# Kernel tuning notes

Measured on AMD Instinct MI355X. Metric: run time of the kernel, lower is better.

Reference implementation:

```python
import jax, jax.numpy as jnp
import numpy as np

NUM_FIELDS = 64
DIM = 128
BATCH = 8192


def setup_inputs() -> dict:
    key = jax.random.key(0)
    k1, k2 = jax.random.split(key)
    inputs = jax.random.normal(k1, (BATCH, NUM_FIELDS * DIM), dtype=jnp.float32)
    field_weights = jax.random.normal(k2, (NUM_FIELDS, NUM_FIELDS), dtype=jnp.float32)
    return {"inputs": inputs, "field_weights": field_weights}


def reference(inputs, field_weights):
    B = inputs.shape[0]
    F = NUM_FIELDS
    D = inputs.shape[1] // F
    x = inputs.reshape(B, F, D)  # [B, F, D]
    # Gram matrix of field vectors: G[b,i,j] = <x_i, x_j>
    gram = jnp.einsum('bid,bjd->bij', x, x)  # [B, F, F]
    # Only pairs (i, j) with i < j contribute (itertools.combinations)
    upper = jnp.triu(jnp.ones((F, F), dtype=inputs.dtype), k=1)
    w = field_weights * upper  # [F, F]
    out = jnp.einsum('bij,ij->b', gram, w)  # sum over masked weighted pairs
    return out[:, None]  # [B, 1]
```

## Files before the change

kernel.cpp:

```cpp
#include <hip/hip_runtime.h>

#define NF 64
#define ND 128

typedef __attribute__((ext_vector_type(8))) short bf16x8;
typedef __attribute__((ext_vector_type(4))) float f32x4;

__device__ __forceinline__ short f2bf(float f) {
    union { float f; unsigned u; } v; v.f = f;
    unsigned r = (v.u + 0x7FFFu + ((v.u >> 16) & 1u)) >> 16;
    return (short)r;
}

__global__ __launch_bounds__(256, 4) void wfi_mfma(const float* __restrict__ x,
                                                   const float* __restrict__ w,
                                                   float* __restrict__ out,
                                                   int Btot) {
    const int tid  = threadIdx.x;
    const int wv   = tid >> 6;
    const int lane = tid & 63;
    const int lo   = lane & 15;
    const int hi   = lane >> 4;
    const int b    = blockIdx.x * 4 + wv;
    if (b >= Btot) return;

    bf16x8 afr[4][2];
#pragma unroll
    for (int jt = 0; jt < 4; ++jt) {
        const int j = jt * 16 + lo;
#pragma unroll
        for (int kt = 0; kt < 2; ++kt) {
#pragma unroll
            for (int e = 0; e < 8; ++e) {
                const int i = kt * 32 + hi * 8 + e;
                const float wval = (i < j) ? w[i * NF + j] : 0.f;
                afr[jt][kt][e] = f2bf(wval);
            }
        }
    }

    const float* __restrict__ xb = x + (size_t)b * (NF * ND);
    float res = 0.f;

#pragma unroll
    for (int dt = 0; dt < 8; ++dt) {
        const int d = dt * 16 + lo;

        bf16x8 bfr[2];
#pragma unroll
        for (int kt = 0; kt < 2; ++kt) {
#pragma unroll
            for (int e = 0; e < 8; ++e) {
                const int i = kt * 32 + hi * 8 + e;
                bfr[kt][e] = f2bf(xb[i * ND + d]);
            }
        }

        f32x4 acc[4] = {{0,0,0,0},{0,0,0,0},{0,0,0,0},{0,0,0,0}};
#pragma unroll
        for (int jt = 0; jt < 4; ++jt) {
#pragma unroll
            for (int kt = 0; kt < 2; ++kt) {
                acc[jt] = __builtin_amdgcn_mfma_f32_16x16x32_bf16(
                    afr[jt][kt], bfr[kt], acc[jt], 0, 0, 0);
            }
        }

#pragma unroll
        for (int jt = 0; jt < 4; ++jt) {
#pragma unroll
            for (int r = 0; r < 4; ++r) {
                const int j = jt * 16 + hi * 4 + r;
                res = fmaf(acc[jt][r], xb[j * ND + d], res);
            }
        }
    }

#pragma unroll
    for (int off = 32; off >= 1; off >>= 1) res += __shfl_down(res, off, 64);
    if (lane == 0) out[b] = res;
}

extern "C" void kernel_launch(void* const* d_in, const int* in_sizes, int n_in,
                              void* d_out, int out_size, void* d_ws, size_t ws_size,
                              hipStream_t stream) {
    const float* x = (const float*)d_in[0];
    const float* w = (const float*)d_in[1];
    float* out = (float*)d_out;

    const int B = in_sizes[0] / (NF * ND);
    dim3 grid((B + 3) / 4);
    dim3 block(256);
    wfi_mfma<<<grid, block, 0, stream>>>(x, w, out, B);
}
```

Measured before the change: 391.7 us.

## Compute upper-triangle Gram tiles via MFMA and contract with weights

Replaces the W·X then dot-with-X formulation with a direct Gram computation: each wave loads its sample's field vectors once as bf16 fragments with vectorized float4 loads, computes only the upper-triangular 16x16 Gram tiles via MFMA over the D dimension, and contracts them with masked weights. This removes the strided scalar loads of x and the second pass over x, and skips lower-triangle tiles. It raises register pressure by holding all 64x128 fragments per wave, and the occupancy hint in launch_bounds is dropped.

```diff
diff --git a/kernel.cpp b/kernel.cpp
--- a/kernel.cpp
+++ b/kernel.cpp
@@ -12,10 +12,10 @@
     return (short)r;
 }
 
-__global__ __launch_bounds__(256, 4) void wfi_mfma(const float* __restrict__ x,
-                                                   const float* __restrict__ w,
-                                                   float* __restrict__ out,
-                                                   int Btot) {
+__global__ __launch_bounds__(256) void wfi_gram(const float* __restrict__ x,
+                                                const float* __restrict__ w,
+                                                float* __restrict__ out,
+                                                int Btot) {
     const int tid  = threadIdx.x;
     const int wv   = tid >> 6;
     const int lane = tid & 63;
@@ -24,54 +24,43 @@
     const int b    = blockIdx.x * 4 + wv;
     if (b >= Btot) return;
 
-    bf16x8 afr[4][2];
+    const float* __restrict__ xb = x + (size_t)b * (NF * ND);
+
+    bf16x8 xf[4][4];
 #pragma unroll
-    for (int jt = 0; jt < 4; ++jt) {
-        const int j = jt * 16 + lo;
+    for (int t = 0; t < 4; ++t) {
+        const float* rowp = xb + (size_t)(t * 16 + lo) * ND + hi * 8;
 #pragma unroll
-        for (int kt = 0; kt < 2; ++kt) {
-#pragma unroll
-            for (int e = 0; e < 8; ++e) {
-                const int i = kt * 32 + hi * 8 + e;
-                const float wval = (i < j) ? w[i * NF + j] : 0.f;
-                afr[jt][kt][e] = f2bf(wval);
-            }
+        for (int kt = 0; kt < 4; ++kt) {
+            const f32x4 a = *(const f32x4*)(rowp + kt * 32);
+            const f32x4 c = *(const f32x4*)(rowp + kt * 32 + 4);
+            bf16x8 f;
+            f[0] = f2bf(a[0]); f[1] = f2bf(a[1]); f[2] = f2bf(a[2]); f[3] = f2bf(a[3]);
+            f[4] = f2bf(c[0]); f[5] = f2bf(c[1]); f[6] = f2bf(c[2]); f[7] = f2bf(c[3]);
+            xf[t][kt] = f;
         }
     }
 
-    const float* __restrict__ xb = x + (size_t)b * (NF * ND);
     float res = 0.f;
-
 #pragma unroll
-    for (int dt = 0; dt < 8; ++dt) {
-        const int d = dt * 16 + lo;
-
-        bf16x8 bfr[2];
+    for (int mt = 0; mt < 4; ++mt) {
 #pragma unroll
-        for (int kt = 0; kt < 2; ++kt) {
+        for (int nt = mt; nt < 4; ++nt) {
+            f32x4 acc = {0.f, 0.f, 0.f, 0.f};
 #pragma unroll
-            for (int e = 0; e < 8; ++e) {
-                const int i = kt * 32 + hi * 8 + e;
-                bfr[kt][e] = f2bf(xb[i * ND + d]);
-            }
-        }
-
-        f32x4 acc[4] = {{0,0,0,0},{0,0,0,0},{0,0,0,0},{0,0,0,0}};
-#pragma unroll
-        for (int jt = 0; jt < 4; ++jt) {
-#pragma unroll
-            for (int kt = 0; kt < 2; ++kt) {
-                acc[jt] = __builtin_amdgcn_mfma_f32_16x16x32_bf16(
-                    afr[jt][kt], bfr[kt], acc[jt], 0, 0, 0);
-            }
-        }
-
-#pragma unroll
-        for (int jt = 0; jt < 4; ++jt) {
+            for (int kt = 0; kt < 4; ++kt)
+                acc = __builtin_amdgcn_mfma_f32_16x16x32_bf16(xf[mt][kt], xf[nt][kt],
+                                                              acc, 0, 0, 0);
 #pragma unroll
             for (int r = 0; r < 4; ++r) {
-                const int j = jt * 16 + hi * 4 + r;
-                res = fmaf(acc[jt][r], xb[j * ND + d], res);
+                const int i = mt * 16 + hi * 4 + r;
+                const int j = nt * 16 + lo;
+                float wij;
+                if (mt == nt)
+                    wij = (hi * 4 + r < lo) ? w[i * NF + j] : 0.f;
+                else
+                    wij = w[i * NF + j];
+                res = fmaf(acc[r], wij, res);
             }
         }
     }
@@ -91,5 +80,5 @@
     const int B = in_sizes[0] / (NF * ND);
     dim3 grid((B + 3) / 4);
     dim3 block(256);
-    wfi_mfma<<<grid, block, 0, stream>>>(x, w, out, B);
+    wfi_gram<<<grid, block, 0, stream>>>(x, w, out, B);
 }
```

Result: faster. 353.4 us (-9.8%).
